# Kernel tuning notes

Measured on AMD Instinct MI355X. Metric: run time of the kernel, lower is better.

The kernel has to match this reference:

```python
import jax, jax.numpy as jnp
import numpy as np

N_NODES = 50000
N_EDGES = 800000
D = 64  # node_dim == edge_dim
NEG_SLOPE = 0.2
EPS = 1e-5


def _lin_params(key, d_in, d_out):
    k1, k2 = jax.random.split(key)
    bound = 1.0 / np.sqrt(d_in)
    W = jax.random.uniform(k1, (d_out, d_in), minval=-bound, maxval=bound, dtype=jnp.float32)
    b = jax.random.uniform(k2, (d_out,), minval=-bound, maxval=bound, dtype=jnp.float32)
    return W, b


def setup_inputs() -> dict:
    key = jax.random.key(0)
    ks = jax.random.split(key, 12)
    V = jax.random.normal(ks[0], (N_NODES, D), dtype=jnp.float32)
    E = jax.random.normal(ks[1], (N_EDGES, D), dtype=jnp.float32)
    src = jax.random.randint(ks[2], (N_EDGES,), 0, N_NODES, dtype=jnp.int32)
    dst = jax.random.randint(ks[3], (N_EDGES,), 0, N_NODES, dtype=jnp.int32)
    pA_w, pA_b = _lin_params(ks[4], D, D)   # NodePooling.A
    pB_w, pB_b = _lin_params(ks[5], D, D)   # NodePooling.B
    mW1, mb1 = _lin_params(ks[6], D, D)     # edge MLP layer 1
    mW2, mb2 = _lin_params(ks[7], D, D)     # edge MLP layer 2
    BW, Bb = _lin_params(ks[8], D, D)       # GenMessage.B (scale)
    CW, Cb = _lin_params(ks[9], D, D)       # GenMessage.C (shift)
    return {"V": V, "E": E, "src": src, "dst": dst,
            "pA_w": pA_w, "pA_b": pA_b, "pB_w": pB_w, "pB_b": pB_b,
            "mW1": mW1, "mb1": mb1, "mW2": mW2, "mb2": mb2,
            "BW": BW, "Bb": Bb, "CW": CW, "Cb": Cb}


def _lrelu(x):
    return jnp.where(x >= 0, x, NEG_SLOPE * x)


def reference(V, E, src, dst, pA_w, pA_b, pB_w, pB_b, mW1, mb1, mW2, mb2, BW, Bb, CW, Cb):
    n = V.shape[0]
    # V = act(V); NodePooling: B(lrelu(A(V)))
    Va = _lrelu(V)
    Vp = _lrelu(Va @ pA_w.T + pA_b) @ pB_w.T + pB_b  # [N, D]
    # edge MLP on edge features (2 Linear+ReLU layers)
    x = jax.nn.relu(E @ mW1.T + mb1)
    x = jax.nn.relu(x @ mW2.T + mb2)                  # [E, D]
    scale = jax.nn.sigmoid(x @ BW.T + Bb)
    shift = x @ CW.T + Cb
    # gathered src features, gated affine message
    M1 = scale * Vp[src] + shift                      # [E, D]
    M2 = M1 * M1
    # segment-mean onto dst (DGL fn.mean); zero for isolated nodes
    deg = jax.ops.segment_sum(jnp.ones((dst.shape[0],), jnp.float32), dst, num_segments=n)
    denom = jnp.maximum(deg, 1.0)[:, None]
    V1 = jax.ops.segment_sum(M1, dst, num_segments=n) / denom
    V2 = jax.ops.segment_sum(M2, dst, num_segments=n) / denom
    return jnp.sqrt(jax.nn.relu(V2 - V1) + EPS)
```

## Files before the change

### kernel.cpp

```cpp
#include <hip/hip_runtime.h>

#define NN 50000
#define NE 800000
#define DDIM 64
#define PADX 68
#define PADS 68
#define NB_SCAN ((NN + 255) / 256)
#define NEG_SLOPE 0.2f
#define EPS_V 1e-5f

typedef short bf16x8 __attribute__((ext_vector_type(8)));
typedef float f32x4 __attribute__((ext_vector_type(4)));

__device__ __forceinline__ float lrelu_f(float x) { return x >= 0.0f ? x : NEG_SLOPE * x; }

__device__ __forceinline__ unsigned short bf16_rn(float x) {
    union { float f; unsigned int u; } c; c.f = x;
    unsigned int r = c.u + 0x7FFF + ((c.u >> 16) & 1);
    return (unsigned short)(r >> 16);
}
__device__ __forceinline__ float bf16_tof(unsigned short h) {
    union { float f; unsigned int u; } c; c.u = ((unsigned int)h) << 16;
    return c.f;
}

__device__ __forceinline__ void split8(const float* __restrict__ v, bf16x8& h, bf16x8& l)
{
    #pragma unroll
    for (int j = 0; j < 8; ++j) {
        unsigned short hh = bf16_rn(v[j]);
        h[j] = (short)hh;
        l[j] = (short)bf16_rn(v[j] - bf16_tof(hh));
    }
}

__device__ __forceinline__ void mma_tile(float acc[16], const float* __restrict__ XT,
                                         const float* __restrict__ Wc, int e0, int f0)
{
    #pragma unroll 4
    for (int kk = 0; kk < DDIM; kk += 4) {
        float4 A0 = *(const float4*)&XT[(kk+0)*PADX + e0];
        float4 A1 = *(const float4*)&XT[(kk+1)*PADX + e0];
        float4 A2 = *(const float4*)&XT[(kk+2)*PADX + e0];
        float4 A3 = *(const float4*)&XT[(kk+3)*PADX + e0];
        float4 B0 = *(const float4*)&Wc[(f0+0)*PADX + kk];
        float4 B1 = *(const float4*)&Wc[(f0+1)*PADX + kk];
        float4 B2 = *(const float4*)&Wc[(f0+2)*PADX + kk];
        float4 B3 = *(const float4*)&Wc[(f0+3)*PADX + kk];
        const float a[4][4] = {{A0.x,A0.y,A0.z,A0.w},{A1.x,A1.y,A1.z,A1.w},
                               {A2.x,A2.y,A2.z,A2.w},{A3.x,A3.y,A3.z,A3.w}};
        const float b[4][4] = {{B0.x,B0.y,B0.z,B0.w},{B1.x,B1.y,B1.z,B1.w},
                               {B2.x,B2.y,B2.z,B2.w},{B3.x,B3.y,B3.z,B3.w}};
        #pragma unroll
        for (int j = 0; j < 4; ++j)
            #pragma unroll
            for (int i = 0; i < 4; ++i)
                #pragma unroll
                for (int q = 0; q < 4; ++q)
                    acc[i*4+j] = fmaf(a[q][i], b[j][q], acc[i*4+j]);
    }
}

__device__ __forceinline__ void load_w_f32(float* __restrict__ Wc, const float* __restrict__ Wg, int tid)
{
    #pragma unroll
    for (int c = 0; c < 4; ++c) {
        int idx = (c << 10) + (tid << 2);
        int f = idx >> 6, k = idx & 63;
        *(float4*)&Wc[f*PADX + k] = *(const float4*)&Wg[idx];
    }
}

__global__ __launch_bounds__(256, 3)
void node_pool_kernel(const float* __restrict__ V,
                      const float* __restrict__ Aw, const float* __restrict__ Ab,
                      const float* __restrict__ Bw, const float* __restrict__ Bbv,
                      float* __restrict__ Vp,
                      const int* __restrict__ dst, int* __restrict__ degi)
{
    __shared__ float Wc[DDIM*PADX];
    __shared__ float XT[DDIM*PADX];
    const int tid = threadIdx.x;
    const int nb = blockIdx.x * 64;
    const int e0 = (tid & 15) << 2;
    const int f0 = (tid >> 4) << 2;

    #pragma unroll
    for (int c = 0; c < 4; ++c) {
        int idx = (c << 10) + (tid << 2);
        int e = idx >> 6, d = idx & 63;
        int row = nb + e; if (row > NN-1) row = NN-1;
        float4 v = *(const float4*)&V[(size_t)row*DDIM + d];
        XT[(d+0)*PADX + e] = lrelu_f(v.x);
        XT[(d+1)*PADX + e] = lrelu_f(v.y);
        XT[(d+2)*PADX + e] = lrelu_f(v.z);
        XT[(d+3)*PADX + e] = lrelu_f(v.w);
    }
    load_w_f32(Wc, Aw, tid);
    __syncthreads();

    float acc[16];
    #pragma unroll
    for (int i = 0; i < 16; ++i) acc[i] = 0.f;
    mma_tile(acc, XT, Wc, e0, f0);
    __syncthreads();

    {
        float4 bv = *(const float4*)&Ab[f0];
        const float ba[4] = {bv.x, bv.y, bv.z, bv.w};
        #pragma unroll
        for (int j = 0; j < 4; ++j) {
            float4 v;
            v.x = lrelu_f(acc[0*4+j] + ba[j]);
            v.y = lrelu_f(acc[1*4+j] + ba[j]);
            v.z = lrelu_f(acc[2*4+j] + ba[j]);
            v.w = lrelu_f(acc[3*4+j] + ba[j]);
            *(float4*)&XT[(f0+j)*PADX + e0] = v;
        }
    }
    load_w_f32(Wc, Bw, tid);
    __syncthreads();

    float acc2[16];
    #pragma unroll
    for (int i = 0; i < 16; ++i) acc2[i] = 0.f;
    mma_tile(acc2, XT, Wc, e0, f0);

    float4 bv = *(const float4*)&Bbv[f0];
    #pragma unroll
    for (int i = 0; i < 4; ++i) {
        int row = nb + e0 + i;
        if (row < NN) {
            float4 o;
            o.x = acc2[i*4+0] + bv.x;
            o.y = acc2[i*4+1] + bv.y;
            o.z = acc2[i*4+2] + bv.z;
            o.w = acc2[i*4+3] + bv.w;
            *(float4*)&Vp[(size_t)row*DDIM + f0] = o;
        }
    }

    const int stride = gridDim.x * 256;
    for (int e = blockIdx.x * 256 + tid; e < NE; e += stride)
        atomicAdd(&degi[dst[e]], 1);
}

__global__ __launch_bounds__(256)
void prep_w_kernel(const float* __restrict__ W1, const float* __restrict__ W2,
                   const float* __restrict__ WB, const float* __restrict__ WC,
                   short* __restrict__ WF)
{
    int gid = blockIdx.x * 256 + threadIdx.x;
    int L = gid >> 12, r = gid & 4095;
    int t = r >> 10, ks = (r >> 9) & 1, lane = (r >> 3) & 63, j = r & 7;
    const float* Ws = (L == 0) ? W1 : (L == 1) ? W2 : (L == 2) ? WB : WC;
    int n = lane & 15, kg = lane >> 4;
    int f = t*16 + n, k = ks*32 + kg*8 + j;
    float v = Ws[f*64 + k];
    unsigned short h = bf16_rn(v);
    unsigned short l = bf16_rn(v - bf16_tof(h));
    int base = L*8192 + ((t*2 + ks)*2)*512 + lane*8 + j;
    WF[base]       = (short)h;
    WF[base + 512] = (short)l;
}

__global__ __launch_bounds__(256)
void scan1_kernel(const int* __restrict__ degi, int* __restrict__ linc, int* __restrict__ bsum)
{
    __shared__ int ws[4];
    const int tid = threadIdx.x;
    const int lane = tid & 63, wv = tid >> 6;
    int i = blockIdx.x * 256 + tid;
    int v = (i < NN) ? degi[i] : 0;
    int sc = v;
    #pragma unroll
    for (int off = 1; off < 64; off <<= 1) {
        int t = __shfl_up(sc, off, 64);
        if (lane >= off) sc += t;
    }
    if (lane == 63) ws[wv] = sc;
    __syncthreads();
    int wb = 0;
    #pragma unroll
    for (int w = 0; w < 4; ++w) if (w < wv) wb += ws[w];
    int incl = sc + wb;
    if (i < NN) linc[i] = incl;
    if (tid == 255) bsum[blockIdx.x] = incl;
}

__global__ __launch_bounds__(256)
void scan23_kernel(const int* __restrict__ degi, const int* __restrict__ linc,
                   const int* __restrict__ bsum, int* __restrict__ curs)
{
    __shared__ int ws[4];
    __shared__ int base_s;
    const int tid = threadIdx.x;
    const int lane = tid & 63, wv = tid >> 6;
    int v = (tid < NB_SCAN) ? bsum[tid] : 0;
    int sc = v;
    #pragma unroll
    for (int off = 1; off < 64; off <<= 1) {
        int t = __shfl_up(sc, off, 64);
        if (lane >= off) sc += t;
    }
    if (lane == 63) ws[wv] = sc;
    __syncthreads();
    int wb = 0;
    #pragma unroll
    for (int w = 0; w < 4; ++w) if (w < wv) wb += ws[w];
    if (tid == blockIdx.x) base_s = sc + wb - v;
    __syncthreads();
    int i = blockIdx.x * 256 + tid;
    if (i < NN) curs[i] = base_s + linc[i] - degi[i];
}

__global__ __launch_bounds__(256)
void scatter_kernel(const int* __restrict__ dst, int* __restrict__ cursor, int* __restrict__ eidx)
{
    int e = blockIdx.x * 256 + threadIdx.x;
    if (e < NE) {
        int p = atomicAdd(&cursor[dst[e]], 1);
        eidx[p] = e;
    }
}

__device__ __forceinline__ void gemm64(const short* __restrict__ WL, int lane,
                                       const bf16x8 ah[2], const bf16x8 al[2], f32x4 acc[4])
{
    #pragma unroll
    for (int ks = 0; ks < 2; ++ks) {
        bf16x8 bh[4], bl[4];
        #pragma unroll
        for (int t = 0; t < 4; ++t) {
            bh[t] = *(const bf16x8*)&WL[(((t*2 + ks)*2 + 0)*64 + lane)*8];
            bl[t] = *(const bf16x8*)&WL[(((t*2 + ks)*2 + 1)*64 + lane)*8];
        }
        #pragma unroll
        for (int t = 0; t < 4; ++t) {
            acc[t] = __builtin_amdgcn_mfma_f32_16x16x32_bf16(al[ks], bh[t], acc[t], 0, 0, 0);
            acc[t] = __builtin_amdgcn_mfma_f32_16x16x32_bf16(ah[ks], bl[t], acc[t], 0, 0, 0);
            acc[t] = __builtin_amdgcn_mfma_f32_16x16x32_bf16(ah[ks], bh[t], acc[t], 0, 0, 0);
        }
    }
}

__device__ __forceinline__ void transpose_frags(float* __restrict__ sw, const f32x4 y[4],
                                                int lane, bf16x8 ah[2], bf16x8 al[2])
{
    const int n = lane & 15, mg = lane >> 4;
    #pragma unroll
    for (int t = 0; t < 4; ++t)
        #pragma unroll
        for (int r = 0; r < 4; ++r)
            sw[(mg*4 + r)*PADS + t*16 + n] = y[t][r];
    __builtin_amdgcn_wave_barrier();
    const int m = lane & 15, kg = lane >> 4;
    float x[16];
    *(float4*)&x[0]  = *(const float4*)&sw[m*PADS + kg*8];
    *(float4*)&x[4]  = *(const float4*)&sw[m*PADS + kg*8 + 4];
    *(float4*)&x[8]  = *(const float4*)&sw[m*PADS + 32 + kg*8];
    *(float4*)&x[12] = *(const float4*)&sw[m*PADS + 32 + kg*8 + 4];
    split8(&x[0], ah[0], al[0]);
    split8(&x[8], ah[1], al[1]);
    __builtin_amdgcn_wave_barrier();
}

__global__ __launch_bounds__(256, 4)
void edge_kernel(const float* __restrict__ Eg,
                 const int* __restrict__ src, const int* __restrict__ dst,
                 const int* __restrict__ eidx,
                 const short* __restrict__ WF,
                 const float* __restrict__ b1, const float* __restrict__ b2,
                 const float* __restrict__ bB, const float* __restrict__ bC,
                 const float* __restrict__ Vp,
                 float* __restrict__ S1, float* __restrict__ S2)
{
    __shared__ float scratch[4 * 16 * PADS];
    __shared__ int aux[4 * 32];

    const int tid = threadIdx.x;
    const int lane = tid & 63, wv = tid >> 6;
    float* sw = scratch + wv * 16 * PADS;
    int* auxw = aux + wv * 32;

    const int ew = blockIdx.x * 64 + wv * 16;
    const int m = lane & 15, kg = lane >> 4;

    int eg = eidx[ew + m];
    if (lane < 16) {
        auxw[lane]      = src[eg];
        auxw[16 + lane] = dst[eg];
    }
    bf16x8 ah[2], al[2];
    {
        const float* er = Eg + (size_t)eg*DDIM + kg*8;
        float x[16];
        *(float4*)&x[0]  = *(const float4*)&er[0];
        *(float4*)&x[4]  = *(const float4*)&er[4];
        *(float4*)&x[8]  = *(const float4*)&er[32];
        *(float4*)&x[12] = *(const float4*)&er[36];
        split8(&x[0], ah[0], al[0]);
        split8(&x[8], ah[1], al[1]);
    }

    const int n = lane & 15, mg = lane >> 4;

    f32x4 acc[4];
    #pragma unroll
    for (int t = 0; t < 4; ++t) acc[t] = (f32x4){0.f, 0.f, 0.f, 0.f};
    gemm64(WF, lane, ah, al, acc);
    #pragma unroll
    for (int t = 0; t < 4; ++t) {
        float b = b1[t*16 + n];
        #pragma unroll
        for (int r = 0; r < 4; ++r) acc[t][r] = fmaxf(acc[t][r] + b, 0.0f);
    }
    transpose_frags(sw, acc, lane, ah, al);

    #pragma unroll
    for (int t = 0; t < 4; ++t) acc[t] = (f32x4){0.f, 0.f, 0.f, 0.f};
    gemm64(WF + 8192, lane, ah, al, acc);
    #pragma unroll
    for (int t = 0; t < 4; ++t) {
        float b = b2[t*16 + n];
        #pragma unroll
        for (int r = 0; r < 4; ++r) acc[t][r] = fmaxf(acc[t][r] + b, 0.0f);
    }
    transpose_frags(sw, acc, lane, ah, al);

    f32x4 accS[4], accH[4];
    #pragma unroll
    for (int t = 0; t < 4; ++t) { accS[t] = (f32x4){0.f,0.f,0.f,0.f}; accH[t] = (f32x4){0.f,0.f,0.f,0.f}; }
    gemm64(WF + 2*8192, lane, ah, al, accS);
    gemm64(WF + 3*8192, lane, ah, al, accH);

    {
        int sn[4];
        #pragma unroll
        for (int r = 0; r < 4; ++r) sn[r] = auxw[mg*4 + r];
        #pragma unroll
        for (int t = 0; t < 4; ++t) {
            const int f = t*16 + n;
            const float bBv = bB[f];
            const float bCv = bC[f];
            #pragma unroll
            for (int r = 0; r < 4; ++r) {
                float vp = Vp[(size_t)sn[r]*DDIM + f];
                float sg = 1.0f / (1.0f + __expf(-(accS[t][r] + bBv)));
                float m1 = fmaf(sg, vp, accH[t][r] + bCv);
                sw[(mg*4 + r)*PADS + f] = m1;
            }
        }
    }
    __builtin_amdgcn_wave_barrier();

    const int f = lane;
    float s1 = 0.f, s2 = 0.f;
    int prev = auxw[16];
    #pragma unroll 4
    for (int e = 0; e < 16; ++e) {
        int dn = auxw[16 + e];
        float m1 = sw[e*PADS + f];
        float m2 = m1 * m1;
        if (dn != prev) {
            atomicAdd(&S1[(size_t)prev*DDIM + f], s1);
            atomicAdd(&S2[(size_t)prev*DDIM + f], s2);
            s1 = 0.f; s2 = 0.f; prev = dn;
        }
        s1 += m1; s2 += m2;
    }
    atomicAdd(&S1[(size_t)prev*DDIM + f], s1);
    atomicAdd(&S2[(size_t)prev*DDIM + f], s2);
}

__global__ __launch_bounds__(256)
void finalize_kernel(const float* __restrict__ S1, const float* __restrict__ S2,
                     const int* __restrict__ degi, float* __restrict__ out)
{
    int gid = blockIdx.x * blockDim.x + threadIdx.x;
    if (gid >= NN*DDIM) return;
    int n = gid >> 6;
    float dn = (float)degi[n];
    dn = dn > 1.0f ? dn : 1.0f;
    float v = (S2[gid] - S1[gid]) / dn;
    out[gid] = sqrtf(fmaxf(v, 0.0f) + EPS_V);
}

extern "C" void kernel_launch(void* const* d_in, const int* in_sizes, int n_in,
                              void* d_out, int out_size, void* d_ws, size_t ws_size,
                              hipStream_t stream) {
    const float* V   = (const float*)d_in[0];
    const float* Eg  = (const float*)d_in[1];
    const int*   src = (const int*)d_in[2];
    const int*   dst = (const int*)d_in[3];
    const float* pAw = (const float*)d_in[4];
    const float* pAb = (const float*)d_in[5];
    const float* pBw = (const float*)d_in[6];
    const float* pBb = (const float*)d_in[7];
    const float* mW1 = (const float*)d_in[8];
    const float* mb1 = (const float*)d_in[9];
    const float* mW2 = (const float*)d_in[10];
    const float* mb2 = (const float*)d_in[11];
    const float* BW  = (const float*)d_in[12];
    const float* Bb  = (const float*)d_in[13];
    const float* CW  = (const float*)d_in[14];
    const float* Cb  = (const float*)d_in[15];
    float* out = (float*)d_out;

    float* ws    = (float*)d_ws;
    float* Vp    = ws;
    float* S1    = ws + (size_t)NN*DDIM;
    float* S2    = ws + (size_t)2*NN*DDIM;
    int*   degi  = (int*)(ws + (size_t)3*NN*DDIM);
    int*   curs  = degi + NN;
    int*   linc  = curs + NN;
    int*   bsum  = linc + NN;
    int*   bbase = bsum + NB_SCAN;
    int*   eidx  = bbase + NB_SCAN;
    short* WF    = (short*)(eidx + NE);

    hipMemsetAsync(S1, 0, (size_t)(2*NN*DDIM + NN) * sizeof(float), stream);

    prep_w_kernel<<<64, 256, 0, stream>>>(mW1, mW2, BW, CW, WF);
    node_pool_kernel<<<(NN + 63)/64, 256, 0, stream>>>(V, pAw, pAb, pBw, pBb, Vp, dst, degi);
    scan1_kernel<<<NB_SCAN, 256, 0, stream>>>(degi, linc, bsum);
    scan23_kernel<<<NB_SCAN, 256, 0, stream>>>(degi, linc, bsum, curs);
    scatter_kernel<<<(NE + 255)/256, 256, 0, stream>>>(dst, curs, eidx);
    edge_kernel<<<NE/64, 256, 0, stream>>>(Eg, src, dst, eidx, WF,
                                           mb1, mb2, Bb, Cb, Vp, S1, S2);
    finalize_kernel<<<(NN*DDIM + 255)/256, 256, 0, stream>>>(S1, S2, degi, out);
}
```

Baseline: 590.5 us.

## Process two 16-edge tiles per wave to reuse weight fragments across MFMAs

Each wave now handles 32 edges as two 16-row tiles, sharing each loaded weight fragment between both tiles' MFMA chains. This halves weight reads from global/L1 per edge and interleaves two independent accumulator chains to hide MFMA latency. Segment runs also get longer, so fewer atomics are issued per edge. The cost is more registers and twice the shared scratch, so occupancy drops (launch bounds go from 4 to 3) and the grid is halved.

```diff
diff --git a/kernel.cpp b/kernel.cpp
--- a/kernel.cpp
+++ b/kernel.cpp
@@ -224,8 +224,10 @@
     }
 }
 
-__device__ __forceinline__ void gemm64(const short* __restrict__ WL, int lane,
-                                       const bf16x8 ah[2], const bf16x8 al[2], f32x4 acc[4])
+__device__ __forceinline__ void gemm64_dual(const short* __restrict__ WL, int lane,
+                                            const bf16x8 ah0[2], const bf16x8 al0[2],
+                                            const bf16x8 ah1[2], const bf16x8 al1[2],
+                                            f32x4 acc0[4], f32x4 acc1[4])
 {
     #pragma unroll
     for (int ks = 0; ks < 2; ++ks) {
@@ -237,35 +239,54 @@
         }
         #pragma unroll
         for (int t = 0; t < 4; ++t) {
-            acc[t] = __builtin_amdgcn_mfma_f32_16x16x32_bf16(al[ks], bh[t], acc[t], 0, 0, 0);
-            acc[t] = __builtin_amdgcn_mfma_f32_16x16x32_bf16(ah[ks], bl[t], acc[t], 0, 0, 0);
-            acc[t] = __builtin_amdgcn_mfma_f32_16x16x32_bf16(ah[ks], bh[t], acc[t], 0, 0, 0);
-        }
-    }
-}
-
-__device__ __forceinline__ void transpose_frags(float* __restrict__ sw, const f32x4 y[4],
-                                                int lane, bf16x8 ah[2], bf16x8 al[2])
+            acc0[t] = __builtin_amdgcn_mfma_f32_16x16x32_bf16(al0[ks], bh[t], acc0[t], 0, 0, 0);
+            acc1[t] = __builtin_amdgcn_mfma_f32_16x16x32_bf16(al1[ks], bh[t], acc1[t], 0, 0, 0);
+            acc0[t] = __builtin_amdgcn_mfma_f32_16x16x32_bf16(ah0[ks], bl[t], acc0[t], 0, 0, 0);
+            acc1[t] = __builtin_amdgcn_mfma_f32_16x16x32_bf16(ah1[ks], bl[t], acc1[t], 0, 0, 0);
+            acc0[t] = __builtin_amdgcn_mfma_f32_16x16x32_bf16(ah0[ks], bh[t], acc0[t], 0, 0, 0);
+            acc1[t] = __builtin_amdgcn_mfma_f32_16x16x32_bf16(ah1[ks], bh[t], acc1[t], 0, 0, 0);
+        }
+    }
+}
+
+__device__ __forceinline__ void transpose_frags_dual(float* __restrict__ sw,
+                                                     const f32x4 y0[4], const f32x4 y1[4],
+                                                     int lane,
+                                                     bf16x8 ah0[2], bf16x8 al0[2],
+                                                     bf16x8 ah1[2], bf16x8 al1[2])
 {
     const int n = lane & 15, mg = lane >> 4;
     #pragma unroll
     for (int t = 0; t < 4; ++t)
         #pragma unroll
-        for (int r = 0; r < 4; ++r)
-            sw[(mg*4 + r)*PADS + t*16 + n] = y[t][r];
+        for (int r = 0; r < 4; ++r) {
+            sw[(mg*4 + r)*PADS + t*16 + n]      = y0[t][r];
+            sw[(16 + mg*4 + r)*PADS + t*16 + n] = y1[t][r];
+        }
     __builtin_amdgcn_wave_barrier();
     const int m = lane & 15, kg = lane >> 4;
-    float x[16];
-    *(float4*)&x[0]  = *(const float4*)&sw[m*PADS + kg*8];
-    *(float4*)&x[4]  = *(const float4*)&sw[m*PADS + kg*8 + 4];
-    *(float4*)&x[8]  = *(const float4*)&sw[m*PADS + 32 + kg*8];
-    *(float4*)&x[12] = *(const float4*)&sw[m*PADS + 32 + kg*8 + 4];
-    split8(&x[0], ah[0], al[0]);
-    split8(&x[8], ah[1], al[1]);
+    {
+        float x[16];
+        *(float4*)&x[0]  = *(const float4*)&sw[m*PADS + kg*8];
+        *(float4*)&x[4]  = *(const float4*)&sw[m*PADS + kg*8 + 4];
+        *(float4*)&x[8]  = *(const float4*)&sw[m*PADS + 32 + kg*8];
+        *(float4*)&x[12] = *(const float4*)&sw[m*PADS + 32 + kg*8 + 4];
+        split8(&x[0], ah0[0], al0[0]);
+        split8(&x[8], ah0[1], al0[1]);
+    }
+    {
+        float x[16];
+        *(float4*)&x[0]  = *(const float4*)&sw[(16+m)*PADS + kg*8];
+        *(float4*)&x[4]  = *(const float4*)&sw[(16+m)*PADS + kg*8 + 4];
+        *(float4*)&x[8]  = *(const float4*)&sw[(16+m)*PADS + 32 + kg*8];
+        *(float4*)&x[12] = *(const float4*)&sw[(16+m)*PADS + 32 + kg*8 + 4];
+        split8(&x[0], ah1[0], al1[0]);
+        split8(&x[8], ah1[1], al1[1]);
+    }
     __builtin_amdgcn_wave_barrier();
 }
 
-__global__ __launch_bounds__(256, 4)
+__global__ __launch_bounds__(256, 3)
 void edge_kernel(const float* __restrict__ Eg,
                  const int* __restrict__ src, const int* __restrict__ dst,
                  const int* __restrict__ eidx,
@@ -275,69 +296,87 @@
                  const float* __restrict__ Vp,
                  float* __restrict__ S1, float* __restrict__ S2)
 {
-    __shared__ float scratch[4 * 16 * PADS];
-    __shared__ int aux[4 * 32];
+    __shared__ float scratch[4 * 32 * PADS];
+    __shared__ int aux[4 * 64];
 
     const int tid = threadIdx.x;
     const int lane = tid & 63, wv = tid >> 6;
-    float* sw = scratch + wv * 16 * PADS;
-    int* auxw = aux + wv * 32;
-
-    const int ew = blockIdx.x * 64 + wv * 16;
+    float* sw = scratch + wv * 32 * PADS;
+    int* auxw = aux + wv * 64;
+
+    const int ew = blockIdx.x * 128 + wv * 32;
     const int m = lane & 15, kg = lane >> 4;
 
-    int eg = eidx[ew + m];
-    if (lane < 16) {
+    if (lane < 32) {
+        int eg = eidx[ew + lane];
         auxw[lane]      = src[eg];
-        auxw[16 + lane] = dst[eg];
-    }
-    bf16x8 ah[2], al[2];
+        auxw[32 + lane] = dst[eg];
+    }
+    bf16x8 ah0[2], al0[2], ah1[2], al1[2];
     {
-        const float* er = Eg + (size_t)eg*DDIM + kg*8;
+        int eg0 = eidx[ew + m];
+        int eg1 = eidx[ew + 16 + m];
+        const float* er0 = Eg + (size_t)eg0*DDIM + kg*8;
+        const float* er1 = Eg + (size_t)eg1*DDIM + kg*8;
         float x[16];
-        *(float4*)&x[0]  = *(const float4*)&er[0];
-        *(float4*)&x[4]  = *(const float4*)&er[4];
-        *(float4*)&x[8]  = *(const float4*)&er[32];
-        *(float4*)&x[12] = *(const float4*)&er[36];
-        split8(&x[0], ah[0], al[0]);
-        split8(&x[8], ah[1], al[1]);
+        *(float4*)&x[0]  = *(const float4*)&er0[0];
+        *(float4*)&x[4]  = *(const float4*)&er0[4];
+        *(float4*)&x[8]  = *(const float4*)&er0[32];
+        *(float4*)&x[12] = *(const float4*)&er0[36];
+        split8(&x[0], ah0[0], al0[0]);
+        split8(&x[8], ah0[1], al0[1]);
+        *(float4*)&x[0]  = *(const float4*)&er1[0];
+        *(float4*)&x[4]  = *(const float4*)&er1[4];
+        *(float4*)&x[8]  = *(const float4*)&er1[32];
+        *(float4*)&x[12] = *(const float4*)&er1[36];
+        split8(&x[0], ah1[0], al1[0]);
+        split8(&x[8], ah1[1], al1[1]);
     }
 
     const int n = lane & 15, mg = lane >> 4;
 
-    f32x4 acc[4];
-    #pragma unroll
-    for (int t = 0; t < 4; ++t) acc[t] = (f32x4){0.f, 0.f, 0.f, 0.f};
-    gemm64(WF, lane, ah, al, acc);
+    f32x4 acc0[4], acc1[4];
+    #pragma unroll
+    for (int t = 0; t < 4; ++t) { acc0[t] = (f32x4){0.f,0.f,0.f,0.f}; acc1[t] = (f32x4){0.f,0.f,0.f,0.f}; }
+    gemm64_dual(WF, lane, ah0, al0, ah1, al1, acc0, acc1);
     #pragma unroll
     for (int t = 0; t < 4; ++t) {
         float b = b1[t*16 + n];
         #pragma unroll
-        for (int r = 0; r < 4; ++r) acc[t][r] = fmaxf(acc[t][r] + b, 0.0f);
-    }
-    transpose_frags(sw, acc, lane, ah, al);
-
-    #pragma unroll
-    for (int t = 0; t < 4; ++t) acc[t] = (f32x4){0.f, 0.f, 0.f, 0.f};
-    gemm64(WF + 8192, lane, ah, al, acc);
+        for (int r = 0; r < 4; ++r) {
+            acc0[t][r] = fmaxf(acc0[t][r] + b, 0.0f);
+            acc1[t][r] = fmaxf(acc1[t][r] + b, 0.0f);
+        }
+    }
+    transpose_frags_dual(sw, acc0, acc1, lane, ah0, al0, ah1, al1);
+
+    #pragma unroll
+    for (int t = 0; t < 4; ++t) { acc0[t] = (f32x4){0.f,0.f,0.f,0.f}; acc1[t] = (f32x4){0.f,0.f,0.f,0.f}; }
+    gemm64_dual(WF + 8192, lane, ah0, al0, ah1, al1, acc0, acc1);
     #pragma unroll
     for (int t = 0; t < 4; ++t) {
         float b = b2[t*16 + n];
         #pragma unroll
-        for (int r = 0; r < 4; ++r) acc[t][r] = fmaxf(acc[t][r] + b, 0.0f);
-    }
-    transpose_frags(sw, acc, lane, ah, al);
-
-    f32x4 accS[4], accH[4];
-    #pragma unroll
-    for (int t = 0; t < 4; ++t) { accS[t] = (f32x4){0.f,0.f,0.f,0.f}; accH[t] = (f32x4){0.f,0.f,0.f,0.f}; }
-    gemm64(WF + 2*8192, lane, ah, al, accS);
-    gemm64(WF + 3*8192, lane, ah, al, accH);
+        for (int r = 0; r < 4; ++r) {
+            acc0[t][r] = fmaxf(acc0[t][r] + b, 0.0f);
+            acc1[t][r] = fmaxf(acc1[t][r] + b, 0.0f);
+        }
+    }
+    transpose_frags_dual(sw, acc0, acc1, lane, ah0, al0, ah1, al1);
+
+    f32x4 accS0[4], accS1[4], accH0[4], accH1[4];
+    #pragma unroll
+    for (int t = 0; t < 4; ++t) {
+        accS0[t] = (f32x4){0.f,0.f,0.f,0.f}; accS1[t] = (f32x4){0.f,0.f,0.f,0.f};
+        accH0[t] = (f32x4){0.f,0.f,0.f,0.f}; accH1[t] = (f32x4){0.f,0.f,0.f,0.f};
+    }
+    gemm64_dual(WF + 2*8192, lane, ah0, al0, ah1, al1, accS0, accS1);
+    gemm64_dual(WF + 3*8192, lane, ah0, al0, ah1, al1, accH0, accH1);
 
     {
-        int sn[4];
-        #pragma unroll
-        for (int r = 0; r < 4; ++r) sn[r] = auxw[mg*4 + r];
+        int sn0[4], sn1[4];
+        #pragma unroll
+        for (int r = 0; r < 4; ++r) { sn0[r] = auxw[mg*4 + r]; sn1[r] = auxw[16 + mg*4 + r]; }
         #pragma unroll
         for (int t = 0; t < 4; ++t) {
             const int f = t*16 + n;
@@ -345,10 +384,12 @@
             const float bCv = bC[f];
             #pragma unroll
             for (int r = 0; r < 4; ++r) {
-                float vp = Vp[(size_t)sn[r]*DDIM + f];
-                float sg = 1.0f / (1.0f + __expf(-(accS[t][r] + bBv)));
-                float m1 = fmaf(sg, vp, accH[t][r] + bCv);
-                sw[(mg*4 + r)*PADS + f] = m1;
+                float vp0 = Vp[(size_t)sn0[r]*DDIM + f];
+                float sg0 = 1.0f / (1.0f + __expf(-(accS0[t][r] + bBv)));
+                sw[(mg*4 + r)*PADS + f] = fmaf(sg0, vp0, accH0[t][r] + bCv);
+                float vp1 = Vp[(size_t)sn1[r]*DDIM + f];
+                float sg1 = 1.0f / (1.0f + __expf(-(accS1[t][r] + bBv)));
+                sw[(16 + mg*4 + r)*PADS + f] = fmaf(sg1, vp1, accH1[t][r] + bCv);
             }
         }
     }
@@ -356,10 +397,10 @@
 
     const int f = lane;
     float s1 = 0.f, s2 = 0.f;
-    int prev = auxw[16];
+    int prev = auxw[32];
     #pragma unroll 4
-    for (int e = 0; e < 16; ++e) {
-        int dn = auxw[16 + e];
+    for (int e = 0; e < 32; ++e) {
+        int dn = auxw[32 + e];
         float m1 = sw[e*PADS + f];
         float m2 = m1 * m1;
         if (dn != prev) {
@@ -426,7 +467,7 @@
     scan1_kernel<<<NB_SCAN, 256, 0, stream>>>(degi, linc, bsum);
     scan23_kernel<<<NB_SCAN, 256, 0, stream>>>(degi, linc, bsum, curs);
     scatter_kernel<<<(NE + 255)/256, 256, 0, stream>>>(dst, curs, eidx);
-    edge_kernel<<<NE/64, 256, 0, stream>>>(Eg, src, dst, eidx, WF,
-                                           mb1, mb2, Bb, Cb, Vp, S1, S2);
+    edge_kernel<<<NE/128, 256, 0, stream>>>(Eg, src, dst, eidx, WF,
+                                            mb1, mb2, Bb, Cb, Vp, S1, S2);
     finalize_kernel<<<(NN*DDIM + 255)/256, 256, 0, stream>>>(S1, S2, degi, out);
 }
```

After: 577.7 us. 2.2% less time.
